# Optimization experiments

Measured on AMD Instinct MI355X. Metric: run time of the kernel, lower is better.

Reference implementation:

```python
import jax, jax.numpy as jnp
import numpy as np

N_NODES = 50000
N_EDGES = 800000
CH = 128
N_GRAPHS = 8
ADD_TO_EDGE_SCORE = 0.5


def edge_scores(x, row, col, lin_w, lin_b, n):
    """Raw edge score via Linear([x_row||x_col]) then scatter-softmax over col."""
    C = x.shape[1]
    # split-weight form of cat([x[row], x[col]]) @ W^T + b (avoids the [E,2C] concat)
    raw = x[row] @ lin_w[0, :C] + x[col] @ lin_w[0, C:] + lin_b[0]  # [E]
    mx = jax.ops.segment_max(raw, col, num_segments=n)
    ex = jnp.exp(raw - mx[col])
    den = jax.ops.segment_sum(ex, col, num_segments=n)
    return ex / (den[col] + 1e-16) + ADD_TO_EDGE_SCORE


def greedy_match_cluster(row_np, col_np, score_np, n):
    """Greedy maximal matching in descending-score order + 2-element clustering."""
    perm = np.argsort(-score_np)
    rows = row_np.tolist()
    cols = col_np.tolist()
    used = np.zeros(n, dtype=bool)
    match = np.zeros(len(rows), dtype=bool)
    for e in perm.tolist():
        r = rows[e]
        c = cols[e]
        if not (used[r] or used[c]):
            match[e] = True
            used[r] = True
            used[c] = True
    cluster = np.arange(n)
    cluster[col_np[match]] = row_np[match]
    _, cluster = np.unique(cluster, return_inverse=True)
    return match, cluster


def setup_inputs() -> dict:
    key = jax.random.key(0)
    k1, k2, k3, k4, k5 = jax.random.split(key, 5)
    x = jax.random.normal(k1, (N_NODES, CH), dtype=jnp.float32)
    edge_index = jax.random.randint(k2, (2, N_EDGES), 0, N_NODES)
    batch = jnp.sort(jax.random.randint(k3, (N_NODES,), 0, N_GRAPHS))
    bound = 1.0 / np.sqrt(2 * CH)
    lin_w = jax.random.uniform(k4, (1, 2 * CH), minval=-bound, maxval=bound, dtype=jnp.float32)
    lin_b = jax.random.uniform(k5, (1,), minval=-bound, maxval=bound, dtype=jnp.float32)
    return {"x": x, "edge_index": edge_index, "batch": batch, "lin_w": lin_w, "lin_b": lin_b}


def reference(x, edge_index, batch, lin_w, lin_b):
    n = x.shape[0]
    row, col = edge_index[0], edge_index[1]
    score = edge_scores(x, row, col, lin_w, lin_b, n)  # [E]

    # sequential greedy matching / cluster relabeling (host side, non-differentiable)
    row_np, col_np = np.asarray(row), np.asarray(col)
    match, cluster_np = greedy_match_cluster(row_np, col_np, np.asarray(score), n)
    c = int(cluster_np.max()) + 1
    match_idx = jnp.asarray(np.nonzero(match)[0])
    cluster = jnp.asarray(cluster_np, dtype=jnp.int32)

    # pooled features scaled by the contracted edge's score (1.0 for singletons)
    new_x = jax.ops.segment_sum(x, cluster, num_segments=c)  # [c, C]
    root = cluster[row[match_idx]]
    new_edge_score = jnp.ones((c,), x.dtype).at[root].set(score[match_idx])
    new_x = new_x * new_edge_score[:, None]

    # coalesce(cluster[edge_index]): sort + dedup
    lin_idx = cluster_np[row_np].astype(np.int64) * c + cluster_np[col_np]
    uniq = np.unique(lin_idx)
    new_edge_index = jnp.asarray(np.stack([uniq // c, uniq % c]).astype(np.int32))

    new_batch = jnp.zeros((c,), dtype=batch.dtype).at[cluster].set(batch)
    return new_x, new_edge_index, new_batch, new_edge_score, cluster
```

## Files before the change

### kernel.cpp

```cpp
#include <hip/hip_runtime.h>

typedef unsigned int u32;
typedef unsigned short u16;
typedef unsigned long long u64;

#define CH_ 128

__device__ __forceinline__ u32 f2ord(float f){
  u32 u = __float_as_uint(f);
  return ((int)u < 0) ? ~u : (u | 0x80000000u);
}
__device__ __forceinline__ float ord2f(u32 u){
  return (u & 0x80000000u) ? __uint_as_float(u & 0x7FFFFFFFu) : __uint_as_float(~u);
}
__device__ __forceinline__ u32 ldu32(const u32* p){
  return __hip_atomic_load(p, __ATOMIC_RELAXED, __HIP_MEMORY_SCOPE_AGENT);
}
__device__ __forceinline__ void stu32(u32* p, u32 v){
  __hip_atomic_store(p, v, __ATOMIC_RELAXED, __HIP_MEMORY_SCOPE_AGENT);
}

__global__ void k_init(u32* hdr, u32* mxbits, double* den, u64* sw,
                       int* craw, int* medge, u32* deg, u32* acur,
                       u32* wpos, u32* offarr, u32 ucap, int N, int E){
  int i0 = blockIdx.x*blockDim.x + threadIdx.x;
  int nt = gridDim.x*blockDim.x;
  for (int v = i0; v < N; v += nt){
    mxbits[v]=0u; den[v]=0.0; sw[v]=0ull; craw[v]=v; medge[v]=-1;
    deg[v]=0u; acur[v]=0u; wpos[v]=0u;
    if (ucap) offarr[v] = (u32)v * ucap;
  }
  if (i0 == 0){
    for (int i = 0; i < 64; i++) hdr[i] = 0u;
    hdr[6] = (u32)N;
    offarr[N] = ucap ? (u32)N*ucap : (u32)(2*E);
  }
}

__global__ void k_dots(const float* __restrict__ x, const float* __restrict__ lw,
                       float* __restrict__ s, float* __restrict__ t, int N){
  int wid = threadIdx.x >> 6, lane = threadIdx.x & 63;
  int node = blockIdx.x*4 + wid;
  if (node >= N) return;
  const float* xr = x + (size_t)node*CH_;
  float xa = xr[lane], xb = xr[64+lane];
  float sv = xa*lw[lane]      + xb*lw[64+lane];
  float tv = xa*lw[128+lane]  + xb*lw[192+lane];
  #pragma unroll
  for (int m = 1; m < 64; m <<= 1){ sv += __shfl_xor(sv, m); tv += __shfl_xor(tv, m); }
  if (lane == 0){ s[node]=sv; t[node]=tv; }
}

__global__ void k_rawmax(const float* __restrict__ s, const float* __restrict__ t,
                         const int* __restrict__ row, const int* __restrict__ col,
                         const float* __restrict__ lb, float* __restrict__ rawex,
                         u32* __restrict__ mxbits, u32* __restrict__ rc,
                         u32* __restrict__ deg, u32 ucap, int E){
  float b = lb[0];
  int i0 = blockIdx.x*blockDim.x + threadIdx.x;
  int nt = gridDim.x*blockDim.x;
  for (int e = i0; e < E; e += nt){
    int r = row[e], c = col[e];
    float raw = (s[r] + t[c]) + b;
    rawex[e] = raw;
    atomicMax(&mxbits[c], f2ord(raw));
    rc[e] = ((u32)r << 16) | (u32)c;
    if (!ucap){
      atomicAdd(&deg[r], 1u);
      atomicAdd(&deg[c], 1u);
    }
  }
}

__global__ void k_exden(const int* __restrict__ col, const u32* __restrict__ mxbits,
                        float* __restrict__ rawex, double* __restrict__ den, int E){
  int i0 = blockIdx.x*blockDim.x + threadIdx.x;
  int nt = gridDim.x*blockDim.x;
  for (int e = i0; e < E; e += nt){
    int c = col[e];
    float ex = expf(rawex[e] - ord2f(mxbits[c]));
    rawex[e] = ex;
    atomicAdd(&den[c], (double)ex);
  }
}

__global__ void k_score(const int* __restrict__ col, float* __restrict__ rawex,
                        const double* __restrict__ den, int E){
  int i0 = blockIdx.x*blockDim.x + threadIdx.x;
  int nt = gridDim.x*blockDim.x;
  for (int e = i0; e < E; e += nt)
    rawex[e] = rawex[e]/(float)den[col[e]] + 0.5f;
}

__global__ void scan_p1(const u32* __restrict__ in, u32* __restrict__ out,
                        u32* __restrict__ bsums, const u32* __restrict__ nptr){
  __shared__ u32 sh[256];
  u32 n = *nptr;
  int t = threadIdx.x;
  u32 i = blockIdx.x*256u + (u32)t;
  u32 v = (i < n) ? in[i] : 0u;
  sh[t] = v; __syncthreads();
  for (int o = 1; o < 256; o <<= 1){
    u32 a = (t >= o) ? sh[t-o] : 0u;
    __syncthreads();
    sh[t] += a;
    __syncthreads();
  }
  if (i < n) out[i] = sh[t] - v;
  if (t == 255) bsums[blockIdx.x] = sh[255];
}
__global__ void scan_p2(u32* bsums, u32* total){
  __shared__ u32 sh[256];
  int t = threadIdx.x;
  u32 v = bsums[t];
  sh[t] = v; __syncthreads();
  for (int o = 1; o < 256; o <<= 1){
    u32 a = (t >= o) ? sh[t-o] : 0u;
    __syncthreads();
    sh[t] += a;
    __syncthreads();
  }
  bsums[t] = sh[t] - v;
  if (t == 255 && total) *total = sh[255];
}
__global__ void scan_p3(u32* out, const u32* __restrict__ bsums, const u32* __restrict__ nptr){
  u32 n = *nptr;
  u32 i = blockIdx.x*256u + threadIdx.x;
  if (i < n) out[i] += bsums[blockIdx.x];
}

__global__ void __launch_bounds__(256)
k_scoreadj(const u32* __restrict__ rc, const float* __restrict__ score,
           const u32* __restrict__ offarr, u32* __restrict__ acur,
           u64* __restrict__ adj, u32 ucap, int ce, int E, int N){
  int xcd   = blockIdx.x & 7;
  int chunk = blockIdx.x >> 3;
  int vspan = (N + 7) >> 3;
  int vlo = xcd * vspan;
  int vhi = vlo + vspan; if (vhi > N) vhi = N;
  int ebeg = chunk * ce;
  int eend = ebeg + ce; if (eend > E) eend = E;
  for (int e = ebeg + (int)threadIdx.x; e < eend; e += 256){
    u32 pk = rc[e];
    int r = (int)(pk >> 16), c = (int)(pk & 0xFFFFu);
    bool wr = (r >= vlo) & (r < vhi);
    bool wc = (c >= vlo) & (c < vhi);
    if (wr | wc){
      u32 sb = __float_as_uint(score[e]) - 0x3F000000u;
      u64 kb = ((u64)sb << 36) | ((u64)(0xFFFFFu - (u32)e) << 16);
      if (wr){
        u32 slot = atomicAdd(&acur[r], 1u);
        if (!ucap || slot < ucap) adj[offarr[r] + slot] = kb | (u32)c;
      }
      if (wc){
        u32 slot = atomicAdd(&acur[c], 1u);
        if (!ucap || slot < ucap) adj[offarr[c] + slot] = kb | (u32)r;
      }
    }
  }
}

__global__ void k_adjsort(const u32* __restrict__ offarr, const u32* __restrict__ acur,
                          u64* __restrict__ adj, u32 ucap, int N){
  __shared__ u64 shk[512];
  int lane = threadIdx.x;
  u32 capn = ucap ? ucap : 0xFFFFFFFFu;
  for (int seg = blockIdx.x; seg < N; seg += gridDim.x){
    u32 base = offarr[seg];
    u32 cnt = acur[seg]; if (cnt > capn) cnt = capn;
    int n = (int)cnt;
    if (n <= 1) continue;
    if (n <= 64){
      u64 v = (lane < n) ? adj[base + lane] : 0ull;
      #pragma unroll
      for (int k2 = 2; k2 <= 64; k2 <<= 1)
        for (int j = k2 >> 1; j > 0; j >>= 1){
          u64 pv = __shfl_xor(v, j);
          bool up  = ((lane & k2) == 0);
          bool low = ((lane & j) == 0);
          u64 mx = v > pv ? v : pv, mn = v > pv ? pv : v;
          v = (up == low) ? mx : mn;
        }
      if (lane < n) adj[base + lane] = v;
    } else {
      int msz = 128; while (msz < n) msz <<= 1;
      for (int i = lane; i < msz; i += 64) shk[i] = (i < n) ? adj[base + i] : 0ull;
      __syncthreads();
      for (int k2 = 2; k2 <= msz; k2 <<= 1){
        for (int j = k2 >> 1; j > 0; j >>= 1){
          for (int i = lane; i < msz; i += 64){
            int ix = i ^ j;
            if (ix > i){
              u64 a = shk[i], b2 = shk[ix];
              bool desc = ((i & k2) == 0);
              if (desc ? (a < b2) : (a > b2)){ shk[i] = b2; shk[ix] = a; }
            }
          }
          __syncthreads();
        }
      }
      for (int i = lane; i < n; i += 64) adj[base+i] = shk[i];
      __syncthreads();
    }
  }
}

__global__ void k_suitor(const u32* __restrict__ rc, const u32* __restrict__ offarr,
                         const u32* __restrict__ acur, const u64* __restrict__ adj,
                         u64* sw, u32* wpos, u32 ucap, int N){
  int i0 = blockIdx.x*blockDim.x + threadIdx.x;
  int nt = gridDim.x*blockDim.x;
  u32 capn = ucap ? ucap : 0xFFFFFFFFu;
  for (int v0 = i0; v0 < N; v0 += nt){
    u32 u = (u32)v0;
    u32 pos = offarr[u];
    u32 cnt = acur[u]; if (cnt > capn) cnt = capn;
    u32 end = pos + cnt;
    while (pos < end){
      u64 k = adj[pos];
      u32 v = (u32)(k & 0xFFFFu);
      pos++;
      if (sw[v] >= k) continue;
      stu32(&wpos[u], pos);
      u64 old = atomicMax((unsigned long long*)&sw[v], (unsigned long long)k);
      if (old >= k) continue;
      if (old == 0ull) break;
      u32 e2 = 0xFFFFFu - (u32)((old >> 16) & 0xFFFFFu);
      u32 p2 = rc[e2];
      u = ((p2 >> 16) == v) ? (p2 & 0xFFFFu) : (p2 >> 16);
      u32 st = offarr[u];
      u32 c2 = acur[u]; if (c2 > capn) c2 = capn;
      end = st + c2;
      u32 wp = ldu32(&wpos[u]);
      pos = (wp > st) ? wp : st;
    }
  }
}

__global__ void k_exroot(const u64* __restrict__ sw, const u32* __restrict__ rc,
                         int* __restrict__ craw, int* __restrict__ medge,
                         u32* __restrict__ rf, int N){
  int v = blockIdx.x*blockDim.x + threadIdx.x;
  if (v >= N) return;
  u64 k = sw[v];
  bool iscol = false;
  if (k != 0ull){
    u32 e = 0xFFFFFu - (u32)((k >> 16) & 0xFFFFFu);
    u32 p = rc[e]; u32 r = p >> 16, c = p & 0xFFFFu;
    if ((u32)v == c && (sw[r] >> 16) == (k >> 16)){
      craw[c] = (int)r; medge[r] = (int)e;
      iscol = (r != c);
    }
  }
  rf[v] = iscol ? 0u : 1u;
}

__global__ void k_clusterzero(const int* __restrict__ craw, const u32* __restrict__ newid,
                              int* __restrict__ clout, float* __restrict__ out, size_t offC,
                              u32* __restrict__ hist, u32* __restrict__ cur2,
                              u32* __restrict__ uniqcnt, int N, int M){
  int i = blockIdx.x*blockDim.x + threadIdx.x;
  if (i < M){ hist[i]=0u; cur2[i]=0u; uniqcnt[i]=0u; }
  if (i < N){
    int cl = (int)newid[craw[i]];
    clout[i] = cl;
    out[offC + i] = (float)cl;
  }
}

__global__ void k_hist(const int* __restrict__ row, const int* __restrict__ clout,
                       u32* __restrict__ hist, int E){
  int i0 = blockIdx.x*blockDim.x + threadIdx.x;
  int nt = gridDim.x*blockDim.x;
  for (int e = i0; e < E; e += nt) atomicAdd(&hist[clout[row[e]]], 1u);
}

__global__ void k_scatter(const int* __restrict__ row, const int* __restrict__ col,
                          const int* __restrict__ clout, const u32* __restrict__ segoff,
                          u32* __restrict__ cur2, u32* __restrict__ ccbuf,
                          const u32* __restrict__ hdr, int E){
  const int P = 4;
  int cnum = (int)hdr[2];
  int span = (cnum + P - 1) / P;
  int i0 = blockIdx.x*blockDim.x + threadIdx.x;
  int nt = gridDim.x*blockDim.x;
  for (int p = 0; p < P; p++){
    int lo = p*span;
    int hi = lo + span; if (hi > cnum) hi = cnum;
    for (int e = i0; e < E; e += nt){
      int cr = clout[row[e]];
      if (cr < lo || cr >= hi) continue;
      u32 pos = segoff[cr] + atomicAdd(&cur2[cr], 1u);
      ccbuf[pos] = (u32)clout[col[e]];
    }
  }
}

__global__ void k_segsort(const u32* __restrict__ hdr, const u32* __restrict__ hist,
                          const u32* __restrict__ segoff, u32* __restrict__ ccbuf,
                          u32* __restrict__ uniqcnt){
  int c = (int)hdr[2];
  __shared__ u32 sh[1024];
  int lane = threadIdx.x;
  for (int seg = blockIdx.x; seg < c; seg += gridDim.x){
    int n = (int)hist[seg];
    if (n <= 0){ if (lane == 0) uniqcnt[seg] = 0u; continue; }
    u32 off = segoff[seg];
    if (n <= 64){
      u32 v = (lane < n) ? ccbuf[off + lane] : 0xFFFFFFFFu;
      #pragma unroll
      for (int k = 2; k <= 64; k <<= 1)
        for (int j = k >> 1; j > 0; j >>= 1){
          u32 p = __shfl_xor(v, j);
          bool up  = ((lane & k) == 0);
          bool low = ((lane & j) == 0);
          u32 mn = v < p ? v : p, mx = v < p ? p : v;
          v = (up == low) ? mn : mx;
        }
      u32 pv = __shfl_up(v, 1);
      bool un = (lane < n) && (lane == 0 || v != pv);
      u64 bal = __ballot(un);
      int cnt = __popcll(bal);
      int rk  = __popcll(bal & ((1ull << lane) - 1ull));
      if (un) ccbuf[off + rk] = v;
      if (lane == 0) uniqcnt[seg] = (u32)cnt;
    } else {
      int nn = n > 1024 ? 1024 : n;
      for (int i = lane; i < nn; i += 64) sh[i] = ccbuf[off + i];
      __syncthreads();
      for (int p = 0; p < nn; p++){
        int st = p & 1;
        for (int i = lane; 2*i + 1 + st < nn; i += 64){
          int a = 2*i + st;
          u32 x0 = sh[a], x1 = sh[a+1];
          if (x0 > x1){ sh[a] = x1; sh[a+1] = x0; }
        }
        __syncthreads();
      }
      if (lane == 0){
        int cnt = 0; u32 prev = 0u;
        for (int i = 0; i < nn; i++){
          u32 xv = sh[i];
          if (i == 0 || xv != prev){ ccbuf[off + cnt] = xv; cnt++; prev = xv; }
        }
        uniqcnt[seg] = (u32)cnt;
      }
      __syncthreads();
    }
  }
}

__global__ void k_out(const u32* __restrict__ hdr, const u32* __restrict__ segoff,
                      const u32* __restrict__ uniqcnt, const u32* __restrict__ uniqoff,
                      const u32* __restrict__ ccbuf, const int* __restrict__ craw,
                      const u32* __restrict__ newid, const int* __restrict__ medge,
                      const int* __restrict__ row, const int* __restrict__ col,
                      const float* __restrict__ score, const int* __restrict__ batch,
                      const float* __restrict__ x, float* __restrict__ out, int N){
  int c = (int)hdr[2]; u32 Ep = hdr[3];
  size_t base = (size_t)c * CH_;
  size_t offB = base + 2ull * (size_t)Ep;
  size_t offS = offB + (size_t)c;
  int gw   = (blockIdx.x*blockDim.x + threadIdx.x) >> 6;
  int lane = threadIdx.x & 63;
  int nw   = (gridDim.x*blockDim.x) >> 6;
  for (int seg = gw; seg < c; seg += nw){
    int cnt = (int)uniqcnt[seg];
    u32 so = segoff[seg], uo = uniqoff[seg];
    for (int j = lane; j < cnt; j += 64){
      u32 cc = ccbuf[so + j];
      out[base + uo + j]              = (float)seg;
      out[base + (size_t)Ep + uo + j] = (float)cc;
    }
  }
  for (int i = gw; i < N; i += nw){
    if (craw[i] != i) continue;
    int j = (int)newid[i];
    int e = medge[i];
    int lo = i, hi = i; float sc = 1.0f;
    if (e >= 0){
      int r = row[e], cc = col[e];
      lo = min(r, cc); hi = max(r, cc);
      sc = score[e];
    }
    float v0 = x[(size_t)lo*CH_ + lane];
    float v1 = x[(size_t)lo*CH_ + 64 + lane];
    if (hi != lo){ v0 += x[(size_t)hi*CH_ + lane]; v1 += x[(size_t)hi*CH_ + 64 + lane]; }
    out[(size_t)j*CH_ + lane]      = v0 * sc;
    out[(size_t)j*CH_ + 64 + lane] = v1 * sc;
    if (lane == 0){
      out[offB + j] = (float)batch[hi];
      out[offS + j] = sc;
    }
  }
}

extern "C" void kernel_launch(void* const* d_in, const int* in_sizes, int n_in,
                              void* d_out, int out_size, void* d_ws, size_t ws_size,
                              hipStream_t stream) {
  const float* x     = (const float*)d_in[0];
  const int*   eidx  = (const int*)d_in[1];
  const int*   batch = (const int*)d_in[2];
  const float* lw    = (const float*)d_in[3];
  const float* lb    = (const float*)d_in[4];

  int N = in_sizes[0] / CH_;
  int E = in_sizes[1] / 2;
  const int* row = eidx;
  const int* col = eidx + E;
  float* out = (float*)d_out;

  char* w = (char*)d_ws;
  size_t off = 0;
  auto carve = [&](size_t bytes) -> void* {
    void* p = w + off;
    off += (bytes + 255) & ~(size_t)255;
    return p;
  };
  u32*    hdr    = (u32*)   carve(256);
  double* den    = (double*)carve((size_t)N*8);
  u64*    sw     = (u64*)   carve((size_t)N*8);
  float*  s      = (float*) carve((size_t)N*4);
  float*  t      = (float*) carve((size_t)N*4);
  float*  rawex  = (float*) carve((size_t)E*4);
  u32*    mxbits = (u32*)   carve((size_t)N*4);
  int*    craw   = (int*)   carve((size_t)N*4);
  u32*    rf     = (u32*)   carve((size_t)N*4);
  u32*    newid  = (u32*)   carve((size_t)N*4);
  int*    medge  = (int*)   carve((size_t)N*4);
  int*    clout  = (int*)   carve((size_t)N*4);
  u32*    rc     = (u32*)   carve((size_t)E*4);
  u32*    deg    = (u32*)   carve((size_t)N*4);
  u32*    acur   = (u32*)   carve((size_t)N*4);
  u32*    wpos   = (u32*)   carve((size_t)N*4);
  u32*    offarr = (u32*)   carve((size_t)(N+1)*4);
  u32*    bsums  = (u32*)   carve(256*4);

  u32 cap = 80;
  size_t adj_b_bytes = ((size_t)N*cap*8 + 255) & ~(size_t)255;
  bool buckets = (off + adj_b_bytes + (1u<<20) <= ws_size);
  u64* adj;
  if (buckets){
    adj = (u64*)carve((size_t)N*cap*8);
  } else {
    cap = 0;
    adj = (u64*)carve((size_t)(2*(size_t)E)*8);
  }
  char* a = (char*)adj;
  size_t aoff = 0;
  auto acarve = [&](size_t bytes) -> void* {
    void* p = a + aoff;
    aoff += (bytes + 255) & ~(size_t)255;
    return p;
  };
  u32* ccbuf   = (u32*)acarve((size_t)E*4);
  u32* hist    = (u32*)acarve((size_t)(N+64)*4);
  u32* segoff  = (u32*)acarve((size_t)(N+64)*4);
  u32* cur2    = (u32*)acarve((size_t)(N+64)*4);
  u32* uniqcnt = (u32*)acarve((size_t)(N+64)*4);
  u32* uniqoff = (u32*)acarve((size_t)(N+64)*4);
  (void)n_in;

  int nbE = (E + 255) / 256;
  int nbN = (N + 255) / 256;
  int ce  = 4096;
  int kch = (E + ce - 1) / ce;

  k_init<<<512, 256, 0, stream>>>(hdr, mxbits, den, sw, craw, medge, deg, acur,
                                  wpos, offarr, cap, N, E);
  k_dots<<<(N + 3)/4, 256, 0, stream>>>(x, lw, s, t, N);
  k_rawmax<<<nbE, 256, 0, stream>>>(s, t, row, col, lb, rawex, mxbits, rc, deg, cap, E);
  k_exden<<<nbE, 256, 0, stream>>>(col, mxbits, rawex, den, E);
  k_score<<<nbE, 256, 0, stream>>>(col, rawex, den, E);

  if (!buckets){
    scan_p1<<<256, 256, 0, stream>>>(deg, offarr, bsums, &hdr[6]);
    scan_p2<<<1, 256, 0, stream>>>(bsums, &hdr[7]);
    scan_p3<<<256, 256, 0, stream>>>(offarr, bsums, &hdr[6]);
  }

  k_scoreadj<<<8*kch, 256, 0, stream>>>(rc, rawex, offarr, acur, adj, cap, ce, E, N);
  k_adjsort<<<4096, 64, 0, stream>>>(offarr, acur, adj, cap, N);
  k_suitor<<<nbN, 256, 0, stream>>>(rc, offarr, acur, adj, sw, wpos, cap, N);
  k_exroot<<<nbN, 256, 0, stream>>>(sw, rc, craw, medge, rf, N);

  scan_p1<<<256, 256, 0, stream>>>(rf, newid, bsums, &hdr[6]);
  scan_p2<<<1, 256, 0, stream>>>(bsums, &hdr[2]);
  scan_p3<<<256, 256, 0, stream>>>(newid, bsums, &hdr[6]);

  k_clusterzero<<<(N + 64 + 255)/256, 256, 0, stream>>>(craw, newid, clout, out,
                                                        (size_t)(out_size - N),
                                                        hist, cur2, uniqcnt, N, N + 64);
  k_hist<<<nbE, 256, 0, stream>>>(row, clout, hist, E);

  scan_p1<<<256, 256, 0, stream>>>(hist, segoff, bsums, &hdr[2]);
  scan_p2<<<1, 256, 0, stream>>>(bsums, &hdr[4]);
  scan_p3<<<256, 256, 0, stream>>>(segoff, bsums, &hdr[2]);

  k_scatter<<<nbE, 256, 0, stream>>>(row, col, clout, segoff, cur2, ccbuf, hdr, E);
  k_segsort<<<4096, 64, 0, stream>>>(hdr, hist, segoff, ccbuf, uniqcnt);

  scan_p1<<<256, 256, 0, stream>>>(uniqcnt, uniqoff, bsums, &hdr[2]);
  scan_p2<<<1, 256, 0, stream>>>(bsums, &hdr[3]);
  scan_p3<<<256, 256, 0, stream>>>(uniqoff, bsums, &hdr[2]);

  k_out<<<4096, 256, 0, stream>>>(hdr, segoff, uniqcnt, uniqoff, ccbuf, craw, newid,
                                  medge, row, col, rawex, batch, x, out, N);
}
```

Baseline: 432.9 us.

## Fuse softmax normalization into adjacency build and output, partition by 16 vertex ranges

Drops the separate k_score pass. The normalized score is now recomputed inline in k_scoreadj and in k_out from the exp values and the per-column denominators, which removes one full read and write pass over the E edges. The adjacency build also splits vertices into 16 ranges instead of 8, which doubles the number of blocks. The cost is redundant divisions and extra gathers of den in each block that touches an edge, plus each edge's rc being read by twice as many blocks.

```diff
diff --git a/kernel.cpp b/kernel.cpp
--- a/kernel.cpp
+++ b/kernel.cpp
@@ -84,14 +84,6 @@
   }
 }
 
-__global__ void k_score(const int* __restrict__ col, float* __restrict__ rawex,
-                        const double* __restrict__ den, int E){
-  int i0 = blockIdx.x*blockDim.x + threadIdx.x;
-  int nt = gridDim.x*blockDim.x;
-  for (int e = i0; e < E; e += nt)
-    rawex[e] = rawex[e]/(float)den[col[e]] + 0.5f;
-}
-
 __global__ void scan_p1(const u32* __restrict__ in, u32* __restrict__ out,
                         u32* __restrict__ bsums, const u32* __restrict__ nptr){
   __shared__ u32 sh[256];
@@ -130,13 +122,14 @@
 }
 
 __global__ void __launch_bounds__(256)
-k_scoreadj(const u32* __restrict__ rc, const float* __restrict__ score,
-           const u32* __restrict__ offarr, u32* __restrict__ acur,
-           u64* __restrict__ adj, u32 ucap, int ce, int E, int N){
-  int xcd   = blockIdx.x & 7;
-  int chunk = blockIdx.x >> 3;
-  int vspan = (N + 7) >> 3;
-  int vlo = xcd * vspan;
+k_scoreadj(const u32* __restrict__ rc, const float* __restrict__ rawex,
+           const double* __restrict__ den, const u32* __restrict__ offarr,
+           u32* __restrict__ acur, u64* __restrict__ adj,
+           u32 ucap, int ce, int E, int N){
+  int rg    = blockIdx.x & 15;
+  int chunk = blockIdx.x >> 4;
+  int vspan = (N + 15) >> 4;
+  int vlo = rg * vspan;
   int vhi = vlo + vspan; if (vhi > N) vhi = N;
   int ebeg = chunk * ce;
   int eend = ebeg + ce; if (eend > E) eend = E;
@@ -146,7 +139,8 @@
     bool wr = (r >= vlo) & (r < vhi);
     bool wc = (c >= vlo) & (c < vhi);
     if (wr | wc){
-      u32 sb = __float_as_uint(score[e]) - 0x3F000000u;
+      float sc = rawex[e]/(float)den[c] + 0.5f;
+      u32 sb = __float_as_uint(sc) - 0x3F000000u;
       u64 kb = ((u64)sb << 36) | ((u64)(0xFFFFFu - (u32)e) << 16);
       if (wr){
         u32 slot = atomicAdd(&acur[r], 1u);
@@ -355,8 +349,9 @@
                       const u32* __restrict__ ccbuf, const int* __restrict__ craw,
                       const u32* __restrict__ newid, const int* __restrict__ medge,
                       const int* __restrict__ row, const int* __restrict__ col,
-                      const float* __restrict__ score, const int* __restrict__ batch,
-                      const float* __restrict__ x, float* __restrict__ out, int N){
+                      const float* __restrict__ rawex, const double* __restrict__ den,
+                      const int* __restrict__ batch, const float* __restrict__ x,
+                      float* __restrict__ out, int N){
   int c = (int)hdr[2]; u32 Ep = hdr[3];
   size_t base = (size_t)c * CH_;
   size_t offB = base + 2ull * (size_t)Ep;
@@ -381,7 +376,7 @@
     if (e >= 0){
       int r = row[e], cc = col[e];
       lo = min(r, cc); hi = max(r, cc);
-      sc = score[e];
+      sc = rawex[e]/(float)den[cc] + 0.5f;
     }
     float v0 = x[(size_t)lo*CH_ + lane];
     float v1 = x[(size_t)lo*CH_ + 64 + lane];
@@ -471,7 +466,6 @@
   k_dots<<<(N + 3)/4, 256, 0, stream>>>(x, lw, s, t, N);
   k_rawmax<<<nbE, 256, 0, stream>>>(s, t, row, col, lb, rawex, mxbits, rc, deg, cap, E);
   k_exden<<<nbE, 256, 0, stream>>>(col, mxbits, rawex, den, E);
-  k_score<<<nbE, 256, 0, stream>>>(col, rawex, den, E);
 
   if (!buckets){
     scan_p1<<<256, 256, 0, stream>>>(deg, offarr, bsums, &hdr[6]);
@@ -479,7 +473,7 @@
     scan_p3<<<256, 256, 0, stream>>>(offarr, bsums, &hdr[6]);
   }
 
-  k_scoreadj<<<8*kch, 256, 0, stream>>>(rc, rawex, offarr, acur, adj, cap, ce, E, N);
+  k_scoreadj<<<16*kch, 256, 0, stream>>>(rc, rawex, den, offarr, acur, adj, cap, ce, E, N);
   k_adjsort<<<4096, 64, 0, stream>>>(offarr, acur, adj, cap, N);
   k_suitor<<<nbN, 256, 0, stream>>>(rc, offarr, acur, adj, sw, wpos, cap, N);
   k_exroot<<<nbN, 256, 0, stream>>>(sw, rc, craw, medge, rf, N);
@@ -505,5 +499,5 @@
   scan_p3<<<256, 256, 0, stream>>>(uniqoff, bsums, &hdr[2]);
 
   k_out<<<4096, 256, 0, stream>>>(hdr, segoff, uniqcnt, uniqoff, ccbuf, craw, newid,
-                                  medge, row, col, rawex, batch, x, out, N);
-}
+                                  medge, row, col, rawex, den, batch, x, out, N);
+}
```

Result: no change. 437.2 us (+1.0%).
